# Performance work log

Measured on AMD Instinct MI355X. Metric: run time of the kernel, lower is better.

The kernel has to match this reference:

```python
import jax, jax.numpy as jnp
import numpy as np
from itertools import combinations

B, F, K, V = 1024, 39, 16, 200000  # batch, fields, embed dim, vocab
EPS = 1e-3  # tf.layers.batch_normalization default epsilon


def setup_inputs() -> dict:
    key = jax.random.key(0)
    ks = jax.random.split(key, 6)
    pairs = np.array(list(combinations(range(F), 2)), dtype=np.int32)   # [741, 2]
    trips = np.array(list(combinations(range(F), 3)), dtype=np.int32)   # [9139, 3]
    P, T = pairs.shape[0], trips.shape[0]
    return {
        "feats": jax.random.randint(ks[0], (B, F), 0, V, dtype=jnp.int32),
        "w": jax.random.normal(ks[1], (V,), dtype=jnp.float32) * 0.01,
        "v": jax.random.normal(ks[2], (V, K), dtype=jnp.float32) * 0.01,
        "b": jnp.zeros((1,), dtype=jnp.float32),
        "gamma2": jnp.ones((P,), dtype=jnp.float32),
        "beta2": jnp.zeros((P,), dtype=jnp.float32),
        "gw2": jax.random.uniform(ks[3], (P,), minval=0.599, maxval=0.601, dtype=jnp.float32),
        "gamma3": jnp.ones((T,), dtype=jnp.float32),
        "beta3": jnp.zeros((T,), dtype=jnp.float32),
        "gw3": jax.random.uniform(ks[4], (T,), minval=0.599, maxval=0.601, dtype=jnp.float32),
        "rows": jnp.asarray(pairs[:, 1]),   # second element of each pair
        "cols": jnp.asarray(pairs[:, 0]),   # first element of each pair
        "i1": jnp.asarray(trips[:, 0]),
        "i2": jnp.asarray(trips[:, 1]),
        "i3": jnp.asarray(trips[:, 2]),
    }


def _batchnorm(x, gamma, beta):
    # training-mode BN over batch axis; x: [B, P]
    m = jnp.mean(x, axis=0)
    var = jnp.mean(jnp.square(x - m), axis=0)
    return (x - m) * jax.lax.rsqrt(var + EPS) * gamma + beta


def reference(feats, w, v, b, gamma2, beta2, gw2, gamma3, beta3, gw3,
              rows, cols, i1, i2, i3):
    xw = w[feats]            # [B, F]  first-order weights
    xv = v[feats]            # [B, F, K] embeddings
    l = jnp.sum(xw, axis=1)  # linear term [B]

    # second-order: gather pair embeddings, multiply, reduce over K
    level2 = jnp.sum(xv[:, rows, :] * xv[:, cols, :], axis=-1)  # [B, P]
    level2 = _batchnorm(level2, gamma2, beta2) * gw2            # soft mask
    fm_out = jnp.sum(level2, axis=-1)                           # [B]

    # third-order: gather triple embeddings
    level3 = jnp.sum(xv[:, i1, :] * xv[:, i2, :] * xv[:, i3, :], axis=-1)  # [B, T]
    level3 = _batchnorm(level3, gamma3, beta3) * gw3
    fm_out2 = jnp.sum(level3, axis=-1)                          # [B]

    logits = l + fm_out + fm_out2 + b[0]                        # [B]
    return logits
```

## Files before the change

### kernel.cpp

```cpp
#include <hip/hip_runtime.h>
#include <hip/hip_fp16.h>
#include <math.h>

#define B_ 1024
#define F_ 39
#define K_ 16
#define P_ 741
#define T_ 9139
#define NC_ 9880
#define EPS_ 1e-3f
#define YSTR 24
#define ESTR 40
#define LS2 9920
#define NSPLIT 8

typedef _Float16 half2v __attribute__((ext_vector_type(2)));

__device__ __forceinline__ float hdot2(unsigned a, unsigned b, float acc) {
    half2v ha = __builtin_bit_cast(half2v, a);
    half2v hb = __builtin_bit_cast(half2v, b);
#if __has_builtin(__builtin_amdgcn_fdot2)
    return __builtin_amdgcn_fdot2(ha, hb, acc, false);
#else
    return acc + (float)ha.x * (float)hb.x + (float)ha.y * (float)hb.y;
#endif
}
__device__ __forceinline__ float f16f(unsigned short h) {
    return __half2float(__builtin_bit_cast(__half, h));
}

__global__ __launch_bounds__(256) void prep_k(const int* __restrict__ rows,
                                              const int* __restrict__ cols,
                                              const int* __restrict__ i1,
                                              const int* __restrict__ i2,
                                              const int* __restrict__ i3,
                                              unsigned* __restrict__ pidx,
                                              float* __restrict__ Cacc) {
    int c = blockIdx.x * 256 + threadIdx.x;
    if (c >= NC_) return;
    if (c == 0) Cacc[0] = 0.f;
    unsigned pk;
    if (c < P_) {
        pk = (unsigned)(cols[c] * ESTR) | ((unsigned)(rows[c] * ESTR) << 11);
    } else {
        int t = c - P_;
        int a = i1[t], b = i2[t], cc = i3[t];
        int p = a * (2 * F_ - 1 - a) / 2 + (b - a - 1);
        pk = (unsigned)(p * YSTR) | ((unsigned)(cc * ESTR) << 15);
    }
    pidx[c] = pk;
}

__global__ __launch_bounds__(512) void levels_k(const int* __restrict__ feats,
                                                const float* __restrict__ v,
                                                const unsigned* __restrict__ pidx,
                                                unsigned short* __restrict__ levels) {
    int b = blockIdx.x;
    int tid = threadIdx.x;
    __shared__ int tok[F_];
    __shared__ __attribute__((aligned(16))) unsigned short emb2[F_ * ESTR];
    __shared__ __attribute__((aligned(16))) unsigned short Y2[P_ * YSTR];

    unsigned short* lrow = levels + (size_t)b * LS2;

    unsigned pk_p0 = (tid < P_) ? pidx[tid] : 0u;
    unsigned pk_p1 = (tid + 512 < P_) ? pidx[tid + 512] : 0u;
    unsigned pkt[18];
#pragma unroll
    for (int i = 0; i < 18; ++i) {
        int t = i * 512 + tid;
        pkt[i] = (t < T_) ? pidx[P_ + t] : 0u;
    }

    if (tid < F_) tok[tid] = feats[b * F_ + tid];
    __syncthreads();
    for (int idx = tid; idx < F_ * K_; idx += 512) {
        int f = idx >> 4, k = idx & 15;
        emb2[f * ESTR + k] = __builtin_bit_cast(unsigned short,
                                 __float2half(v[(size_t)tok[f] * K_ + k]));
    }
    __syncthreads();

#pragma unroll 1
    for (int pp = 0; pp < 2; ++pp) {
        int p = pp * 512 + tid;
        if (p < P_) {
            unsigned pk = pp == 0 ? pk_p0 : pk_p1;
            int o1 = (int)(pk & 2047u);
            int o2 = (int)((pk >> 11) & 2047u);
            uint4 ua0 = *(const uint4*)&emb2[o1];
            uint4 ua1 = *(const uint4*)&emb2[o1 + 8];
            uint4 uc0 = *(const uint4*)&emb2[o2];
            uint4 uc1 = *(const uint4*)&emb2[o2 + 8];
            float s = 0.f;
            uint4 y0, y1;
#define PKMUL(dst, a, c) {                                                    \
            half2v _a = __builtin_bit_cast(half2v, a);                        \
            half2v _c = __builtin_bit_cast(half2v, c);                        \
            half2v _y = _a * _c;                                              \
            dst = __builtin_bit_cast(unsigned, _y);                           \
            s = hdot2(a, c, s); }
            PKMUL(y0.x, ua0.x, uc0.x); PKMUL(y0.y, ua0.y, uc0.y);
            PKMUL(y0.z, ua0.z, uc0.z); PKMUL(y0.w, ua0.w, uc0.w);
            PKMUL(y1.x, ua1.x, uc1.x); PKMUL(y1.y, ua1.y, uc1.y);
            PKMUL(y1.z, ua1.z, uc1.z); PKMUL(y1.w, ua1.w, uc1.w);
#undef PKMUL
            *(uint4*)&Y2[p * YSTR] = y0;
            *(uint4*)&Y2[p * YSTR + 8] = y1;
            lrow[p] = __builtin_bit_cast(unsigned short, __float2half(s));
        }
    }
    __syncthreads();

#pragma unroll 3
    for (int i = 0; i < 18; ++i) {
        int t = i * 512 + tid;
        if (t < T_) {
            unsigned pk = pkt[i];
            int yb = (int)(pk & 32767u);
            int o3 = (int)(pk >> 15);
            uint4 uy0 = *(const uint4*)&Y2[yb];
            uint4 uy1 = *(const uint4*)&Y2[yb + 8];
            uint4 ue0 = *(const uint4*)&emb2[o3];
            uint4 ue1 = *(const uint4*)&emb2[o3 + 8];
            float s = 0.f;
            s = hdot2(uy0.x, ue0.x, s); s = hdot2(uy0.y, ue0.y, s);
            s = hdot2(uy0.z, ue0.z, s); s = hdot2(uy0.w, ue0.w, s);
            s = hdot2(uy1.x, ue1.x, s); s = hdot2(uy1.y, ue1.y, s);
            s = hdot2(uy1.z, ue1.z, s);
            s = hdot2(uy1.w, ue1.w, s);
            lrow[P_ + t] = __builtin_bit_cast(unsigned short, __float2half(s));
        }
    }
}

__global__ __launch_bounds__(256) void stats2_k(const unsigned short* __restrict__ levels,
                                                float* __restrict__ psum,
                                                float* __restrict__ psumsq) {
    int col = blockIdx.x * 256 + threadIdx.x;
    if (col >= NC_) return;
    int sy = blockIdx.y;
    const unsigned short* p = levels + (size_t)(sy * (B_ / NSPLIT)) * LS2 + col;
    float a0 = 0.f, a1 = 0.f, a2 = 0.f, a3 = 0.f;
    float q0 = 0.f, q1 = 0.f, q2 = 0.f, q3 = 0.f;
#pragma unroll 4
    for (int r = 0; r < B_ / NSPLIT; r += 4) {
        float x0 = f16f(p[(size_t)(r + 0) * LS2]);
        float x1 = f16f(p[(size_t)(r + 1) * LS2]);
        float x2 = f16f(p[(size_t)(r + 2) * LS2]);
        float x3 = f16f(p[(size_t)(r + 3) * LS2]);
        a0 += x0; q0 += x0 * x0;
        a1 += x1; q1 += x1 * x1;
        a2 += x2; q2 += x2 * x2;
        a3 += x3; q3 += x3 * x3;
    }
    psum[sy * NC_ + col]   = (a0 + a1) + (a2 + a3);
    psumsq[sy * NC_ + col] = (q0 + q1) + (q2 + q3);
}

__global__ __launch_bounds__(256) void finalize_k(const float* __restrict__ psum,
                                                  const float* __restrict__ psumsq,
                                                  const float* __restrict__ gamma2,
                                                  const float* __restrict__ beta2,
                                                  const float* __restrict__ gw2,
                                                  const float* __restrict__ gamma3,
                                                  const float* __restrict__ beta3,
                                                  const float* __restrict__ gw3,
                                                  float* __restrict__ scale,
                                                  float* __restrict__ Cacc) {
    int col = blockIdx.x * 256 + threadIdx.x;
    float c = 0.f;
    if (col < NC_) {
        float s1 = 0.f, s2 = 0.f;
#pragma unroll
        for (int sy = 0; sy < NSPLIT; ++sy) {
            s1 += psum[sy * NC_ + col];
            s2 += psumsq[sy * NC_ + col];
        }
        float mean = s1 * (1.0f / B_);
        float var  = s2 * (1.0f / B_) - mean * mean;
        float inv  = 1.0f / sqrtf(var + EPS_);
        float g, be, gw;
        if (col < P_) {
            g = gamma2[col]; be = beta2[col]; gw = gw2[col];
        } else {
            int t = col - P_;
            g = gamma3[t]; be = beta3[t]; gw = gw3[t];
        }
        scale[col] = gw * g * inv;
        c = gw * (be - g * inv * mean);
    }
    __shared__ float red[256];
    red[threadIdx.x] = c;
    __syncthreads();
    for (int s = 128; s > 0; s >>= 1) {
        if (threadIdx.x < s) red[threadIdx.x] += red[threadIdx.x + s];
        __syncthreads();
    }
    if (threadIdx.x == 0) atomicAdd(Cacc, red[0]);
}

__global__ __launch_bounds__(256) void out_k(const unsigned short* __restrict__ levels,
                                             const float* __restrict__ scale,
                                             const int* __restrict__ feats,
                                             const float* __restrict__ w,
                                             const float* __restrict__ Cacc,
                                             const float* __restrict__ bias,
                                             float* __restrict__ out) {
    int b = blockIdx.x, tid = threadIdx.x;
    const uint4* lv = (const uint4*)(levels + (size_t)b * LS2);
    float acc = 0.f;
    for (int idx = tid; idx < 1235; idx += 256) {
        uint4 u = lv[idx];
        float4 sa = *(const float4*)&scale[idx * 8];
        float4 sb = *(const float4*)&scale[idx * 8 + 4];
        float2 f0 = __half22float2(__builtin_bit_cast(__half2, u.x));
        float2 f1 = __half22float2(__builtin_bit_cast(__half2, u.y));
        float2 f2 = __half22float2(__builtin_bit_cast(__half2, u.z));
        float2 f3 = __half22float2(__builtin_bit_cast(__half2, u.w));
        acc += sa.x * f0.x + sa.y * f0.y + sa.z * f1.x + sa.w * f1.y;
        acc += sb.x * f2.x + sb.y * f2.y + sb.z * f3.x + sb.w * f3.y;
    }
    if (tid < F_) acc += w[feats[b * F_ + tid]];
    __shared__ float red[256];
    red[tid] = acc;
    __syncthreads();
    for (int s = 128; s > 0; s >>= 1) {
        if (tid < s) red[tid] += red[tid + s];
        __syncthreads();
    }
    if (tid == 0) out[b] = red[0] + Cacc[0] + bias[0];
}

extern "C" void kernel_launch(void* const* d_in, const int* in_sizes, int n_in,
                              void* d_out, int out_size, void* d_ws, size_t ws_size,
                              hipStream_t stream) {
    const int*   feats  = (const int*)d_in[0];
    const float* w      = (const float*)d_in[1];
    const float* v      = (const float*)d_in[2];
    const float* bias   = (const float*)d_in[3];
    const float* gamma2 = (const float*)d_in[4];
    const float* beta2  = (const float*)d_in[5];
    const float* gw2    = (const float*)d_in[6];
    const float* gamma3 = (const float*)d_in[7];
    const float* beta3  = (const float*)d_in[8];
    const float* gw3    = (const float*)d_in[9];
    const int*   rows   = (const int*)d_in[10];
    const int*   cols   = (const int*)d_in[11];
    const int*   i1     = (const int*)d_in[12];
    const int*   i2     = (const int*)d_in[13];
    const int*   i3     = (const int*)d_in[14];
    float*       out    = (float*)d_out;
    float*       ws     = (float*)d_ws;

    float*          scale    = ws;
    float*          psum     = ws + 9880;
    float*          psumsq   = ws + 88920;
    float*          Cacc     = ws + 167960;
    unsigned*       pidx     = (unsigned*)(ws + 168064);
    unsigned short* levels   = (unsigned short*)(ws + 177984);

    prep_k<<<(NC_ + 255) / 256, 256, 0, stream>>>(rows, cols, i1, i2, i3, pidx, Cacc);
    levels_k<<<B_, 512, 0, stream>>>(feats, v, pidx, levels);
    stats2_k<<<dim3((NC_ + 255) / 256, NSPLIT), 256, 0, stream>>>(levels, psum, psumsq);
    finalize_k<<<(NC_ + 255) / 256, 256, 0, stream>>>(psum, psumsq,
                                                      gamma2, beta2, gw2,
                                                      gamma3, beta3, gw3, scale, Cacc);
    out_k<<<B_, 256, 0, stream>>>(levels, scale, feats, w, Cacc, bias, out);
}
```

Measured before the change: 123.3 us.

## Restructure triple-level layout for contiguous per-thread work, vectorized stats and fp16 scale

Each thread now computes 18 consecutive triples, so it can reuse the pair product Y when consecutive triples share a pair. Results are packed into shared memory and written to global with aligned 16-byte stores at a padded offset (TBASE=744). The stats kernel reads 8 halves per uint4 with a finer batch split. The scale vector is stored in fp16 so out_k can use packed fdot2. Y stride shrinks to 16, which may add LDS bank conflicts, and the fp16 scale lowers precision.

```diff
diff --git a/kernel.cpp b/kernel.cpp
--- a/kernel.cpp
+++ b/kernel.cpp
@@ -9,10 +9,12 @@
 #define T_ 9139
 #define NC_ 9880
 #define EPS_ 1e-3f
-#define YSTR 24
+#define YSTR 16
 #define ESTR 40
+#define TBASE 744
 #define LS2 9920
-#define NSPLIT 8
+#define NG 1240
+#define NSPLIT 32
 
 typedef _Float16 half2v __attribute__((ext_vector_type(2)));
 
@@ -27,6 +29,9 @@
 }
 __device__ __forceinline__ float f16f(unsigned short h) {
     return __half2float(__builtin_bit_cast(__half, h));
+}
+__device__ __forceinline__ unsigned short hbits(float x) {
+    return __builtin_bit_cast(unsigned short, __float2half(x));
 }
 
 __global__ __launch_bounds__(256) void prep_k(const int* __restrict__ rows,
@@ -39,16 +44,14 @@
     int c = blockIdx.x * 256 + threadIdx.x;
     if (c >= NC_) return;
     if (c == 0) Cacc[0] = 0.f;
-    unsigned pk;
     if (c < P_) {
-        pk = (unsigned)(cols[c] * ESTR) | ((unsigned)(rows[c] * ESTR) << 11);
+        pidx[c] = (unsigned)(cols[c] * ESTR) | ((unsigned)(rows[c] * ESTR) << 11);
     } else {
         int t = c - P_;
         int a = i1[t], b = i2[t], cc = i3[t];
         int p = a * (2 * F_ - 1 - a) / 2 + (b - a - 1);
-        pk = (unsigned)(p * YSTR) | ((unsigned)(cc * ESTR) << 15);
-    }
-    pidx[c] = pk;
+        pidx[TBASE + t] = (unsigned)(p * YSTR) | ((unsigned)(cc * ESTR) << 15);
+    }
 }
 
 __global__ __launch_bounds__(512) void levels_k(const int* __restrict__ feats,
@@ -59,29 +62,31 @@
     int tid = threadIdx.x;
     __shared__ int tok[F_];
     __shared__ __attribute__((aligned(16))) unsigned short emb2[F_ * ESTR];
-    __shared__ __attribute__((aligned(16))) unsigned short Y2[P_ * YSTR];
+    __shared__ __attribute__((aligned(16))) unsigned short region[P_ * YSTR];
+    unsigned short* Y2 = region;
+    unsigned* bufw = (unsigned*)region;
 
     unsigned short* lrow = levels + (size_t)b * LS2;
 
     unsigned pk_p0 = (tid < P_) ? pidx[tid] : 0u;
     unsigned pk_p1 = (tid + 512 < P_) ? pidx[tid + 512] : 0u;
+    int t0 = 18 * tid;
     unsigned pkt[18];
-#pragma unroll
-    for (int i = 0; i < 18; ++i) {
-        int t = i * 512 + tid;
-        pkt[i] = (t < T_) ? pidx[P_ + t] : 0u;
+    {
+        const uint2* tp = (const uint2*)(pidx + TBASE + t0);
+#pragma unroll
+        for (int j = 0; j < 9; ++j) { uint2 u = tp[j]; pkt[2*j] = u.x; pkt[2*j+1] = u.y; }
     }
 
     if (tid < F_) tok[tid] = feats[b * F_ + tid];
     __syncthreads();
     for (int idx = tid; idx < F_ * K_; idx += 512) {
         int f = idx >> 4, k = idx & 15;
-        emb2[f * ESTR + k] = __builtin_bit_cast(unsigned short,
-                                 __float2half(v[(size_t)tok[f] * K_ + k]));
-    }
-    __syncthreads();
-
-#pragma unroll 1
+        emb2[f * ESTR + k] = hbits(v[(size_t)tok[f] * K_ + k]);
+    }
+    __syncthreads();
+
+#pragma unroll
     for (int pp = 0; pp < 2; ++pp) {
         int p = pp * 512 + tid;
         if (p < P_) {
@@ -107,55 +112,80 @@
 #undef PKMUL
             *(uint4*)&Y2[p * YSTR] = y0;
             *(uint4*)&Y2[p * YSTR + 8] = y1;
-            lrow[p] = __builtin_bit_cast(unsigned short, __float2half(s));
-        }
-    }
-    __syncthreads();
-
-#pragma unroll 3
-    for (int i = 0; i < 18; ++i) {
-        int t = i * 512 + tid;
+            lrow[p] = hbits(s);
+        }
+    }
+    __syncthreads();
+
+    unsigned cur = 0xFFFFFFFFu;
+    uint4 uy0, uy1;
+    unsigned resp[9];
+#pragma unroll
+    for (int j = 0; j < 18; ++j) {
+        int t = t0 + j;
+        unsigned short r = 0;
         if (t < T_) {
-            unsigned pk = pkt[i];
-            int yb = (int)(pk & 32767u);
+            unsigned pk = pkt[j];
+            unsigned yb = pk & 32767u;
             int o3 = (int)(pk >> 15);
-            uint4 uy0 = *(const uint4*)&Y2[yb];
-            uint4 uy1 = *(const uint4*)&Y2[yb + 8];
+            if (yb != cur) {
+                cur = yb;
+                uy0 = *(const uint4*)&Y2[yb];
+                uy1 = *(const uint4*)&Y2[yb + 8];
+            }
             uint4 ue0 = *(const uint4*)&emb2[o3];
             uint4 ue1 = *(const uint4*)&emb2[o3 + 8];
             float s = 0.f;
             s = hdot2(uy0.x, ue0.x, s); s = hdot2(uy0.y, ue0.y, s);
             s = hdot2(uy0.z, ue0.z, s); s = hdot2(uy0.w, ue0.w, s);
             s = hdot2(uy1.x, ue1.x, s); s = hdot2(uy1.y, ue1.y, s);
-            s = hdot2(uy1.z, ue1.z, s);
-            s = hdot2(uy1.w, ue1.w, s);
-            lrow[P_ + t] = __builtin_bit_cast(unsigned short, __float2half(s));
-        }
-    }
+            s = hdot2(uy1.z, ue1.z, s); s = hdot2(uy1.w, ue1.w, s);
+            r = hbits(s);
+        }
+        if (j & 1) resp[j >> 1] |= ((unsigned)r) << 16;
+        else       resp[j >> 1] = (unsigned)r;
+    }
+    __syncthreads();
+
+#pragma unroll
+    for (int j = 0; j < 9; ++j)
+        bufw[9 * tid + j] = resp[j];
+    if (tid < 3) lrow[P_ + tid] = 0;
+    __syncthreads();
+
+    uint4* dst = (uint4*)(lrow + TBASE);
+    const uint4* src = (const uint4*)bufw;
+    for (int idx = tid; idx < 1147; idx += 512)
+        dst[idx] = src[idx];
 }
 
 __global__ __launch_bounds__(256) void stats2_k(const unsigned short* __restrict__ levels,
                                                 float* __restrict__ psum,
                                                 float* __restrict__ psumsq) {
-    int col = blockIdx.x * 256 + threadIdx.x;
-    if (col >= NC_) return;
+    int g = blockIdx.x * 256 + threadIdx.x;
+    if (g >= NG) return;
     int sy = blockIdx.y;
-    const unsigned short* p = levels + (size_t)(sy * (B_ / NSPLIT)) * LS2 + col;
-    float a0 = 0.f, a1 = 0.f, a2 = 0.f, a3 = 0.f;
-    float q0 = 0.f, q1 = 0.f, q2 = 0.f, q3 = 0.f;
+    const uint4* p = (const uint4*)levels + (size_t)(sy * (B_ / NSPLIT)) * NG + g;
+    float s1[8] = {0,0,0,0,0,0,0,0};
+    float s2[8] = {0,0,0,0,0,0,0,0};
 #pragma unroll 4
-    for (int r = 0; r < B_ / NSPLIT; r += 4) {
-        float x0 = f16f(p[(size_t)(r + 0) * LS2]);
-        float x1 = f16f(p[(size_t)(r + 1) * LS2]);
-        float x2 = f16f(p[(size_t)(r + 2) * LS2]);
-        float x3 = f16f(p[(size_t)(r + 3) * LS2]);
-        a0 += x0; q0 += x0 * x0;
-        a1 += x1; q1 += x1 * x1;
-        a2 += x2; q2 += x2 * x2;
-        a3 += x3; q3 += x3 * x3;
-    }
-    psum[sy * NC_ + col]   = (a0 + a1) + (a2 + a3);
-    psumsq[sy * NC_ + col] = (q0 + q1) + (q2 + q3);
+    for (int r = 0; r < B_ / NSPLIT; ++r) {
+        uint4 u = p[(size_t)r * NG];
+        unsigned uu[4] = {u.x, u.y, u.z, u.w};
+#pragma unroll
+        for (int q = 0; q < 4; ++q) {
+            float x0 = __uint_as_float((uu[q] & 0xffffu) ? 0 : 0);
+            (void)x0;
+            float a = f16f((unsigned short)(uu[q] & 0xffffu));
+            float c = f16f((unsigned short)(uu[q] >> 16));
+            s1[2*q]   += a; s2[2*q]   += a * a;
+            s1[2*q+1] += c; s2[2*q+1] += c * c;
+        }
+    }
+    float* d1 = psum   + (size_t)sy * LS2 + g * 8;
+    float* d2 = psumsq + (size_t)sy * LS2 + g * 8;
+#pragma unroll
+    for (int k = 0; k < 8; ++k) { d1[k] = s1[k]; d2[k] = s2[k]; }
 }
 
 __global__ __launch_bounds__(256) void finalize_k(const float* __restrict__ psum,
@@ -166,28 +196,28 @@
                                                   const float* __restrict__ gamma3,
                                                   const float* __restrict__ beta3,
                                                   const float* __restrict__ gw3,
-                                                  float* __restrict__ scale,
+                                                  unsigned short* __restrict__ scale_h,
                                                   float* __restrict__ Cacc) {
     int col = blockIdx.x * 256 + threadIdx.x;
     float c = 0.f;
-    if (col < NC_) {
+    if (col < LS2) {
         float s1 = 0.f, s2 = 0.f;
-#pragma unroll
+#pragma unroll 8
         for (int sy = 0; sy < NSPLIT; ++sy) {
-            s1 += psum[sy * NC_ + col];
-            s2 += psumsq[sy * NC_ + col];
+            s1 += psum[(size_t)sy * LS2 + col];
+            s2 += psumsq[(size_t)sy * LS2 + col];
+        }
+        float g = 0.f, be = 0.f, gw = 0.f;
+        if (col < P_) {
+            g = gamma2[col]; be = beta2[col]; gw = gw2[col];
+        } else if (col >= TBASE && col < TBASE + T_) {
+            int t = col - TBASE;
+            g = gamma3[t]; be = beta3[t]; gw = gw3[t];
         }
         float mean = s1 * (1.0f / B_);
         float var  = s2 * (1.0f / B_) - mean * mean;
         float inv  = 1.0f / sqrtf(var + EPS_);
-        float g, be, gw;
-        if (col < P_) {
-            g = gamma2[col]; be = beta2[col]; gw = gw2[col];
-        } else {
-            int t = col - P_;
-            g = gamma3[t]; be = beta3[t]; gw = gw3[t];
-        }
-        scale[col] = gw * g * inv;
+        scale_h[col] = hbits(gw * g * inv);
         c = gw * (be - g * inv * mean);
     }
     __shared__ float red[256];
@@ -201,7 +231,7 @@
 }
 
 __global__ __launch_bounds__(256) void out_k(const unsigned short* __restrict__ levels,
-                                             const float* __restrict__ scale,
+                                             const unsigned short* __restrict__ scale_h,
                                              const int* __restrict__ feats,
                                              const float* __restrict__ w,
                                              const float* __restrict__ Cacc,
@@ -209,17 +239,15 @@
                                              float* __restrict__ out) {
     int b = blockIdx.x, tid = threadIdx.x;
     const uint4* lv = (const uint4*)(levels + (size_t)b * LS2);
+    const uint4* sv = (const uint4*)scale_h;
     float acc = 0.f;
-    for (int idx = tid; idx < 1235; idx += 256) {
+    for (int idx = tid; idx < NG; idx += 256) {
         uint4 u = lv[idx];
-        float4 sa = *(const float4*)&scale[idx * 8];
-        float4 sb = *(const float4*)&scale[idx * 8 + 4];
-        float2 f0 = __half22float2(__builtin_bit_cast(__half2, u.x));
-        float2 f1 = __half22float2(__builtin_bit_cast(__half2, u.y));
-        float2 f2 = __half22float2(__builtin_bit_cast(__half2, u.z));
-        float2 f3 = __half22float2(__builtin_bit_cast(__half2, u.w));
-        acc += sa.x * f0.x + sa.y * f0.y + sa.z * f1.x + sa.w * f1.y;
-        acc += sb.x * f2.x + sb.y * f2.y + sb.z * f3.x + sb.w * f3.y;
+        uint4 s = sv[idx];
+        acc = hdot2(u.x, s.x, acc);
+        acc = hdot2(u.y, s.y, acc);
+        acc = hdot2(u.z, s.z, acc);
+        acc = hdot2(u.w, s.w, acc);
     }
     if (tid < F_) acc += w[feats[b * F_ + tid]];
     __shared__ float red[256];
@@ -253,18 +281,18 @@
     float*       out    = (float*)d_out;
     float*       ws     = (float*)d_ws;
 
-    float*          scale    = ws;
-    float*          psum     = ws + 9880;
-    float*          psumsq   = ws + 88920;
-    float*          Cacc     = ws + 167960;
-    unsigned*       pidx     = (unsigned*)(ws + 168064);
-    unsigned short* levels   = (unsigned short*)(ws + 177984);
+    float*          psum    = ws;
+    float*          psumsq  = ws + 317440;
+    float*          Cacc    = ws + 634880;
+    unsigned short* scale_h = (unsigned short*)(ws + 634944);
+    unsigned*       pidx    = (unsigned*)(ws + 639936);
+    unsigned short* levels  = (unsigned short*)(ws + 649984);
 
     prep_k<<<(NC_ + 255) / 256, 256, 0, stream>>>(rows, cols, i1, i2, i3, pidx, Cacc);
     levels_k<<<B_, 512, 0, stream>>>(feats, v, pidx, levels);
-    stats2_k<<<dim3((NC_ + 255) / 256, NSPLIT), 256, 0, stream>>>(levels, psum, psumsq);
-    finalize_k<<<(NC_ + 255) / 256, 256, 0, stream>>>(psum, psumsq,
+    stats2_k<<<dim3((NG + 255) / 256, NSPLIT), 256, 0, stream>>>(levels, psum, psumsq);
+    finalize_k<<<(LS2 + 255) / 256, 256, 0, stream>>>(psum, psumsq,
                                                       gamma2, beta2, gw2,
-                                                      gamma3, beta3, gw3, scale, Cacc);
-    out_k<<<B_, 256, 0, stream>>>(levels, scale, feats, w, Cacc, bias, out);
-}
+                                                      gamma3, beta3, gw3, scale_h, Cacc);
+    out_k<<<B_, 256, 0, stream>>>(levels, scale_h, feats, w, Cacc, bias, out);
+}
```

New measurement: 128.6 us. 1.04x slower.

## Vectorize BN stats reads, store fp16 scales, use fdot2 in output reduction

Applied to the files above, without the earlier changes.

The batch-norm statistics kernel now reads eight fp16 columns per thread with 16-byte loads instead of one 2-byte load per column, and the batch split rises from 8 to 16 to keep enough blocks in flight. The per-column scale is stored in fp16, and the output kernel does packed fp16 dot products (fdot2) against it, halving scale traffic and cutting conversion work. The workspace layout is rearranged to fit the larger partial-sum buffers. The pair loop in the levels kernel is also fully unrolled. The trade-offs are some precision loss from rounding the scale to fp16 and more register pressure from the 16 accumulators.

```diff
diff --git a/kernel.cpp b/kernel.cpp
--- a/kernel.cpp
+++ b/kernel.cpp
@@ -12,7 +12,9 @@
 #define YSTR 24
 #define ESTR 40
 #define LS2 9920
-#define NSPLIT 8
+#define NGD 1235
+#define NGR 1240
+#define NSPLIT 16
 
 typedef _Float16 half2v __attribute__((ext_vector_type(2)));
 
@@ -27,6 +29,9 @@
 }
 __device__ __forceinline__ float f16f(unsigned short h) {
     return __half2float(__builtin_bit_cast(__half, h));
+}
+__device__ __forceinline__ unsigned short hbits(float x) {
+    return __builtin_bit_cast(unsigned short, __float2half(x));
 }
 
 __global__ __launch_bounds__(256) void prep_k(const int* __restrict__ rows,
@@ -76,12 +81,11 @@
     __syncthreads();
     for (int idx = tid; idx < F_ * K_; idx += 512) {
         int f = idx >> 4, k = idx & 15;
-        emb2[f * ESTR + k] = __builtin_bit_cast(unsigned short,
-                                 __float2half(v[(size_t)tok[f] * K_ + k]));
-    }
-    __syncthreads();
-
-#pragma unroll 1
+        emb2[f * ESTR + k] = hbits(v[(size_t)tok[f] * K_ + k]);
+    }
+    __syncthreads();
+
+#pragma unroll
     for (int pp = 0; pp < 2; ++pp) {
         int p = pp * 512 + tid;
         if (p < P_) {
@@ -107,7 +111,7 @@
 #undef PKMUL
             *(uint4*)&Y2[p * YSTR] = y0;
             *(uint4*)&Y2[p * YSTR + 8] = y1;
-            lrow[p] = __builtin_bit_cast(unsigned short, __float2half(s));
+            lrow[p] = hbits(s);
         }
     }
     __syncthreads();
@@ -127,9 +131,8 @@
             s = hdot2(uy0.x, ue0.x, s); s = hdot2(uy0.y, ue0.y, s);
             s = hdot2(uy0.z, ue0.z, s); s = hdot2(uy0.w, ue0.w, s);
             s = hdot2(uy1.x, ue1.x, s); s = hdot2(uy1.y, ue1.y, s);
-            s = hdot2(uy1.z, ue1.z, s);
-            s = hdot2(uy1.w, ue1.w, s);
-            lrow[P_ + t] = __builtin_bit_cast(unsigned short, __float2half(s));
+            s = hdot2(uy1.z, ue1.z, s); s = hdot2(uy1.w, ue1.w, s);
+            lrow[P_ + t] = hbits(s);
         }
     }
 }
@@ -137,25 +140,28 @@
 __global__ __launch_bounds__(256) void stats2_k(const unsigned short* __restrict__ levels,
                                                 float* __restrict__ psum,
                                                 float* __restrict__ psumsq) {
-    int col = blockIdx.x * 256 + threadIdx.x;
-    if (col >= NC_) return;
+    int g = blockIdx.x * 256 + threadIdx.x;
+    if (g >= NGD) return;
     int sy = blockIdx.y;
-    const unsigned short* p = levels + (size_t)(sy * (B_ / NSPLIT)) * LS2 + col;
-    float a0 = 0.f, a1 = 0.f, a2 = 0.f, a3 = 0.f;
-    float q0 = 0.f, q1 = 0.f, q2 = 0.f, q3 = 0.f;
+    const uint4* p = (const uint4*)levels + (size_t)(sy * (B_ / NSPLIT)) * NGR + g;
+    float s1[8] = {0,0,0,0,0,0,0,0};
+    float s2[8] = {0,0,0,0,0,0,0,0};
 #pragma unroll 4
-    for (int r = 0; r < B_ / NSPLIT; r += 4) {
-        float x0 = f16f(p[(size_t)(r + 0) * LS2]);
-        float x1 = f16f(p[(size_t)(r + 1) * LS2]);
-        float x2 = f16f(p[(size_t)(r + 2) * LS2]);
-        float x3 = f16f(p[(size_t)(r + 3) * LS2]);
-        a0 += x0; q0 += x0 * x0;
-        a1 += x1; q1 += x1 * x1;
-        a2 += x2; q2 += x2 * x2;
-        a3 += x3; q3 += x3 * x3;
-    }
-    psum[sy * NC_ + col]   = (a0 + a1) + (a2 + a3);
-    psumsq[sy * NC_ + col] = (q0 + q1) + (q2 + q3);
+    for (int r = 0; r < B_ / NSPLIT; ++r) {
+        uint4 u = p[(size_t)r * NGR];
+        unsigned uu[4] = {u.x, u.y, u.z, u.w};
+#pragma unroll
+        for (int q = 0; q < 4; ++q) {
+            float a = f16f((unsigned short)(uu[q] & 0xffffu));
+            float c = f16f((unsigned short)(uu[q] >> 16));
+            s1[2*q]   += a; s2[2*q]   += a * a;
+            s1[2*q+1] += c; s2[2*q+1] += c * c;
+        }
+    }
+    float* d1 = psum   + (size_t)sy * NC_ + g * 8;
+    float* d2 = psumsq + (size_t)sy * NC_ + g * 8;
+#pragma unroll
+    for (int k = 0; k < 8; ++k) { d1[k] = s1[k]; d2[k] = s2[k]; }
 }
 
 __global__ __launch_bounds__(256) void finalize_k(const float* __restrict__ psum,
@@ -166,16 +172,16 @@
                                                   const float* __restrict__ gamma3,
                                                   const float* __restrict__ beta3,
                                                   const float* __restrict__ gw3,
-                                                  float* __restrict__ scale,
+                                                  unsigned short* __restrict__ scale_h,
                                                   float* __restrict__ Cacc) {
     int col = blockIdx.x * 256 + threadIdx.x;
     float c = 0.f;
     if (col < NC_) {
         float s1 = 0.f, s2 = 0.f;
-#pragma unroll
+#pragma unroll 8
         for (int sy = 0; sy < NSPLIT; ++sy) {
-            s1 += psum[sy * NC_ + col];
-            s2 += psumsq[sy * NC_ + col];
+            s1 += psum[(size_t)sy * NC_ + col];
+            s2 += psumsq[(size_t)sy * NC_ + col];
         }
         float mean = s1 * (1.0f / B_);
         float var  = s2 * (1.0f / B_) - mean * mean;
@@ -187,7 +193,7 @@
             int t = col - P_;
             g = gamma3[t]; be = beta3[t]; gw = gw3[t];
         }
-        scale[col] = gw * g * inv;
+        scale_h[col] = hbits(gw * g * inv);
         c = gw * (be - g * inv * mean);
     }
     __shared__ float red[256];
@@ -201,7 +207,7 @@
 }
 
 __global__ __launch_bounds__(256) void out_k(const unsigned short* __restrict__ levels,
-                                             const float* __restrict__ scale,
+                                             const unsigned short* __restrict__ scale_h,
                                              const int* __restrict__ feats,
                                              const float* __restrict__ w,
                                              const float* __restrict__ Cacc,
@@ -209,17 +215,15 @@
                                              float* __restrict__ out) {
     int b = blockIdx.x, tid = threadIdx.x;
     const uint4* lv = (const uint4*)(levels + (size_t)b * LS2);
+    const uint4* sv = (const uint4*)scale_h;
     float acc = 0.f;
-    for (int idx = tid; idx < 1235; idx += 256) {
+    for (int idx = tid; idx < NGD; idx += 256) {
         uint4 u = lv[idx];
-        float4 sa = *(const float4*)&scale[idx * 8];
-        float4 sb = *(const float4*)&scale[idx * 8 + 4];
-        float2 f0 = __half22float2(__builtin_bit_cast(__half2, u.x));
-        float2 f1 = __half22float2(__builtin_bit_cast(__half2, u.y));
-        float2 f2 = __half22float2(__builtin_bit_cast(__half2, u.z));
-        float2 f3 = __half22float2(__builtin_bit_cast(__half2, u.w));
-        acc += sa.x * f0.x + sa.y * f0.y + sa.z * f1.x + sa.w * f1.y;
-        acc += sb.x * f2.x + sb.y * f2.y + sb.z * f3.x + sb.w * f3.y;
+        uint4 s = sv[idx];
+        acc = hdot2(u.x, s.x, acc);
+        acc = hdot2(u.y, s.y, acc);
+        acc = hdot2(u.z, s.z, acc);
+        acc = hdot2(u.w, s.w, acc);
     }
     if (tid < F_) acc += w[feats[b * F_ + tid]];
     __shared__ float red[256];
@@ -253,18 +257,18 @@
     float*       out    = (float*)d_out;
     float*       ws     = (float*)d_ws;
 
-    float*          scale    = ws;
-    float*          psum     = ws + 9880;
-    float*          psumsq   = ws + 88920;
-    float*          Cacc     = ws + 167960;
-    unsigned*       pidx     = (unsigned*)(ws + 168064);
-    unsigned short* levels   = (unsigned short*)(ws + 177984);
+    float*          psum    = ws;
+    float*          psumsq  = ws + 158080;
+    float*          Cacc    = ws + 316160;
+    unsigned short* scale_h = (unsigned short*)(ws + 316168);
+    unsigned*       pidx    = (unsigned*)(ws + 321112);
+    unsigned short* levels  = (unsigned short*)(ws + 330996);
 
     prep_k<<<(NC_ + 255) / 256, 256, 0, stream>>>(rows, cols, i1, i2, i3, pidx, Cacc);
     levels_k<<<B_, 512, 0, stream>>>(feats, v, pidx, levels);
-    stats2_k<<<dim3((NC_ + 255) / 256, NSPLIT), 256, 0, stream>>>(levels, psum, psumsq);
+    stats2_k<<<dim3((NGD + 255) / 256, NSPLIT), 256, 0, stream>>>(levels, psum, psumsq);
     finalize_k<<<(NC_ + 255) / 256, 256, 0, stream>>>(psum, psumsq,
                                                       gamma2, beta2, gw2,
-                                                      gamma3, beta3, gw3, scale, Cacc);
-    out_k<<<B_, 256, 0, stream>>>(levels, scale, feats, w, Cacc, bias, out);
-}
+                                                      gamma3, beta3, gw3, scale_h, Cacc);
+    out_k<<<B_, 256, 0, stream>>>(levels, scale_h, feats, w, Cacc, bias, out);
+}
```

Result: slower. 129.0 us (+4.6%).
